# Performance work log

Measured on AMD Instinct MI355X. Metric: run time of the kernel, lower is better.

The kernel has to match this reference:

```python
import jax, jax.numpy as jnp
import numpy as np

NUM_EMBEDDINGS = 512
EMBEDDING_DIM = 64
BETA = 0.25


def setup_inputs() -> dict:
    key = jax.random.key(0)
    k1, k2 = jax.random.split(key)
    latent_z = jax.random.normal(k1, (32, EMBEDDING_DIM, 64, 64), dtype=jnp.float32)
    # nn.Embedding init: uniform(-1/K, 1/K)
    scale = 1.0 / NUM_EMBEDDINGS
    embedding = jax.random.uniform(k2, (NUM_EMBEDDINGS, EMBEDDING_DIM), dtype=jnp.float32,
                                   minval=-scale, maxval=scale)
    return {"latent_z": latent_z, "embedding": embedding}


def reference(latent_z, embedding):
    # [B, C, H, W] -> [B, H, W, C]
    z = jnp.transpose(latent_z, (0, 2, 3, 1))
    B, H, W, D = z.shape
    flat_z = z.reshape(-1, D)  # [N, D]

    # squared L2 distances via expansion: ||z||^2 + ||e||^2 - 2 z.e
    dist = (jnp.sum(flat_z ** 2, axis=1, keepdims=True)
            + jnp.sum(embedding ** 2, axis=1)
            - 2.0 * flat_z @ embedding.T)  # [N, K]

    idx = jnp.argmin(dist, axis=1)  # [N]
    encodings = jax.nn.one_hot(idx, NUM_EMBEDDINGS, dtype=flat_z.dtype)  # [N, K]

    # gather codes (same math as one_hot @ embedding)
    quantized = embedding[idx].reshape(B, H, W, D)

    quant_loss = (jnp.mean((jax.lax.stop_gradient(quantized) - z) ** 2)
                  + BETA * jnp.mean((quantized - jax.lax.stop_gradient(z)) ** 2))

    # straight-through estimator
    quantized_st = z + jax.lax.stop_gradient(quantized - z)

    mean_enc = jnp.mean(encodings, axis=0)
    perplexity = jnp.exp(-jnp.sum(mean_enc * jnp.log(mean_enc + 1e-10)))

    quantized_out = jnp.transpose(quantized_st, (0, 3, 1, 2))  # back to [B, C, H, W]
    return quant_loss, quantized_out, perplexity, encodings, idx[:, None]
```

## Files before the change

kernel.cpp:

```cpp
#include <hip/hip_runtime.h>
#include <math.h>

#define NPIX   131072
#define KCODES 512
#define DIM    64
#define HW     4096
#define CHW    262144
#define NBLK   1024

#define O_Q    1ll
#define O_PERP 8388609ll
#define O_ENC  8388610ll
#define O_IDX  75497474ll


__device__ __forceinline__ float np_sumsq64(const float (&x)[64]) {
#pragma clang fp contract(off)
  float r0 = x[0]*x[0], r1 = x[1]*x[1], r2 = x[2]*x[2], r3 = x[3]*x[3];
  float r4 = x[4]*x[4], r5 = x[5]*x[5], r6 = x[6]*x[6], r7 = x[7]*x[7];
#pragma unroll
  for (int i = 8; i < 64; i += 8) {
    r0 += x[i+0]*x[i+0];
    r1 += x[i+1]*x[i+1];
    r2 += x[i+2]*x[i+2];
    r3 += x[i+3]*x[i+3];
    r4 += x[i+4]*x[i+4];
    r5 += x[i+5]*x[i+5];
    r6 += x[i+6]*x[i+6];
    r7 += x[i+7]*x[i+7];
  }
  return ((r0+r1)+(r2+r3))+((r4+r5)+(r6+r7));
}

__global__ void vq_prep(const float* __restrict__ emb, float* __restrict__ ws) {
  const int t = threadIdx.x;
  if (t == 0) ws[0] = 0.0f;
  ((unsigned*)ws)[1 + t] = 0u;
  float x[64];
  const float* e = emb + t * DIM;
#pragma unroll
  for (int d = 0; d < 64; ++d) x[d] = e[d];
  ws[513 + t] = np_sumsq64(x);
}


__device__ __forceinline__ void et_prefetch8(const float* __restrict__ emb,
                                             int g, int ec, int eh, float4& p0) {
  const float* er = emb + (size_t)(256 * (g >> 3) + ec) * 64
                        + 8 * (g & 7) + 4 * eh;
  p0 = *(const float4*)er;
}

__device__ __forceinline__ void et_write8(float* __restrict__ ETb,
                                          const float4& p0, int eh, int ec) {
  const float tmp[4] = {p0.x, p0.y, p0.z, p0.w};
#pragma unroll
  for (int dl = 0; dl < 4; ++dl) ETb[(4 * eh + dl) * 256 + ec] = tmp[dl];
}

__device__ __forceinline__ void enc_zero(float2* __restrict__ encb, int batch, int t) {
  const float2 zz = make_float2(0.0f, 0.0f);
#pragma unroll
  for (int u = 0; u < 8; ++u)
    encb[(size_t)batch * 4096 + u * 512 + t] = zz;
}

__device__ __forceinline__ void dl_loop8(const float* __restrict__ ETb,
                                         const float* __restrict__ zl,
                                         int sdim, int pi, int ci,
                                         float (&acc)[8][8]) {
#pragma unroll 2
  for (int dl = 0; dl < 8; ++dl) {
    const float* zp = &zl[(sdim + dl) * 128 + 8 * pi];
    const float4 za0 = *(const float4*)(zp + 0);
    const float4 za1 = *(const float4*)(zp + 4);
    const float* ep = &ETb[dl * 256 + 4 * ci];
    const float4 e0 = *(const float4*)(ep + 0);
    const float4 e1 = *(const float4*)(ep + 128);
    const float zr[8] = {za0.x, za0.y, za0.z, za0.w,
                         za1.x, za1.y, za1.z, za1.w};
    const float er_[8] = {e0.x, e0.y, e0.z, e0.w,
                          e1.x, e1.y, e1.z, e1.w};
#pragma unroll
    for (int j = 0; j < 8; ++j)
#pragma unroll
      for (int c = 0; c < 8; ++c)
        acc[j][c] = fmaf(zr[j], er_[c], acc[j][c]);
  }
}

__device__ __forceinline__ void dist_phase(int Hh, int ci, int pi,
                                           const float (&acc)[8][8],
                                           const float* __restrict__ esq_l,
                                           const float* __restrict__ zsq_l,
                                           float (&bd)[8], int (&bk)[8]) {
#pragma unroll
  for (int q = 0; q < 2; ++q)
#pragma unroll
    for (int r = 0; r < 4; ++r) {
      const int k = 256 * Hh + 128 * q + 4 * ci + r;
      const float eq = esq_l[k];
#pragma unroll
      for (int j = 0; j < 8; ++j) {
        const float dist = (zsq_l[8 * pi + j] + eq) - 2.0f * acc[j][4 * q + r];
        if (dist < bd[j]) { bd[j] = dist; bk[j] = k; }
      }
    }
}

__global__ __launch_bounds__(512, 4)
void vq_main(
    const float* __restrict__ z, const float* __restrict__ emb,
    float* __restrict__ out, float* __restrict__ ws)
{
  __shared__ float ET_s[2][8 * 256];
  __shared__ float z_l[64 * 128];
  __shared__ float esq_l[512];
  __shared__ float zsq_l[128];
  __shared__ int   ridx_l[128];
  __shared__ float wsum[8];

  const int t   = threadIdx.x;
  const int ci  = t & 31;
  const int pi  = t >> 5;
  const int blk = blockIdx.x;
  const int n0  = blk * 128;
  const int b   = n0 >> 12;
  const int hw0 = n0 & 4095;
  const float* zg = z + (size_t)b * CHW + hw0;

  esq_l[t] = ws[513 + t];

  {
    const int i     = t & 31;
    const int dbase = t >> 5;
#pragma unroll
    for (int r = 0; r < 4; ++r) {
      const int d = dbase + 16 * r;
      *(float4*)&z_l[d * 128 + 4 * i] = *(const float4*)(zg + (size_t)d * HW + 4 * i);
    }
  }

  const int ec = t & 255;
  const int eh = t >> 8;
  float4 p0;
  et_prefetch8(emb, 0, ec, eh, p0);

  __syncthreads();

  if (t < 128) {
    float x[64];
#pragma unroll
    for (int d = 0; d < 64; ++d) x[d] = z_l[d * 128 + t];
    zsq_l[t] = np_sumsq64(x);
  }

  et_write8(&ET_s[0][0], p0, eh, ec);
  et_prefetch8(emb, 1, ec, eh, p0);

  __syncthreads();

  float bd[8];
  int   bk[8];
#pragma unroll
  for (int j = 0; j < 8; ++j) { bd[j] = INFINITY; bk[j] = 0; }
  float acc[8][8];
#pragma unroll
  for (int j = 0; j < 8; ++j)
#pragma unroll
    for (int c = 0; c < 8; ++c) acc[j][c] = 0.0f;

  float2* encb = (float2*)(out + O_ENC) + (size_t)n0 * 256;

  for (int g = 0; g < 16; ++g) {
    if (g < 15) et_write8(&ET_s[(g + 1) & 1][0], p0, eh, ec);
    if (g < 14) et_prefetch8(emb, g + 2, ec, eh, p0);
    if (!(g & 1)) enc_zero(encb, g >> 1, t);
    dl_loop8(&ET_s[g & 1][0], z_l, 8 * (g & 7), pi, ci, acc);
    if ((g & 7) == 7) {
      dist_phase(g >> 3, ci, pi, acc, esq_l, zsq_l, bd, bk);
      if (g == 7) {
#pragma unroll
        for (int j = 0; j < 8; ++j)
#pragma unroll
          for (int c = 0; c < 8; ++c) acc[j][c] = 0.0f;
      }
    }
    __syncthreads();
  }

#pragma unroll
  for (int m = 16; m >= 1; m >>= 1) {
#pragma unroll
    for (int j = 0; j < 8; ++j) {
      const float od = __shfl_xor(bd[j], m, 64);
      const int   ok = __shfl_xor(bk[j], m, 64);
      if (od < bd[j] || (od == bd[j] && ok < bk[j])) { bd[j] = od; bk[j] = ok; }
    }
  }
  if (ci == 0) {
#pragma unroll
    for (int j = 0; j < 8; ++j) ridx_l[8 * pi + j] = bk[j];
  }
  __syncthreads();

  if (t < 128) {
    const int k = ridx_l[t];
    out[O_IDX + n0 + t] = (float)k;
    atomicAdd((unsigned*)ws + 1 + k, 1u);
    out[O_ENC + (size_t)(n0 + t) * 512 + k] = 1.0f;
  }

  {
    const int px = t & 127;
    const int dq = t >> 7;
    const int k  = ridx_l[px];
    const float* e0 = emb + ((size_t)k << 6);
    float* q0 = out + O_Q + (size_t)b * CHW + hw0 + px;
    float lsum = 0.0f;
#pragma unroll
    for (int j = 0; j < 16; ++j) {
      const int d = dq * 16 + j;
      const float ev = e0[d];
      const float df = ev - z_l[d * 128 + px];
      lsum = fmaf(df, df, lsum);
      q0[(size_t)d * HW] = ev;
    }
#pragma unroll
    for (int off = 32; off > 0; off >>= 1) lsum += __shfl_down(lsum, off, 64);
    if ((t & 63) == 0) wsum[t >> 6] = lsum;
  }
  __syncthreads();
  if (t == 0)
    atomicAdd(ws, ((wsum[0] + wsum[1]) + (wsum[2] + wsum[3])) +
                  ((wsum[4] + wsum[5]) + (wsum[6] + wsum[7])));
}

__global__ void vq_fin(float* __restrict__ out, const float* __restrict__ ws) {
  __shared__ float red[8];
  const int t = threadIdx.x;
  const unsigned* counts = (const unsigned*)ws + 1;
  const float p = (float)counts[t] * (1.0f / 131072.0f);
  float h = p * logf(p + 1e-10f);
#pragma unroll
  for (int off = 32; off > 0; off >>= 1) h += __shfl_down(h, off, 64);
  if ((t & 63) == 0) red[t >> 6] = h;
  __syncthreads();
  if (t == 0) {
    float H = 0.0f;
#pragma unroll
    for (int w = 0; w < 8; ++w) H += red[w];
    out[O_PERP] = expf(-H);
    out[0] = 1.25f * ws[0] * (1.0f / 8388608.0f);
  }
}

extern "C" void kernel_launch(void* const* d_in, const int* in_sizes, int n_in,
                              void* d_out, int out_size, void* d_ws, size_t ws_size,
                              hipStream_t stream) {
  const float* z   = (const float*)d_in[0];
  const float* emb = (const float*)d_in[1];
  float* out = (float*)d_out;
  float* ws  = (float*)d_ws;

  vq_prep<<<1, 512, 0, stream>>>(emb, ws);
  vq_main<<<NBLK, 512, 0, stream>>>(z, emb, out, ws);
  vq_fin<<<1, 512, 0, stream>>>(out, ws);
}
```

Before: 445.4 us.

## Stage transposed codebook in workspace and load tiles via direct global-to-LDS loads

The prep kernel now also writes a transposed copy of the embedding into the workspace. The main kernel fills the z tile and the codebook tiles with global_load_lds DMA straight into shared memory, instead of going through registers and scattered LDS stores. The codebook K-step is doubled to 16 dims per stage, halving the number of barriers and loop trips, and s_setprio is raised around the FMA loop. In exchange there is more LDS per block, which may reduce occupancy, and the kernel now depends on async LDS load semantics. The diff ends mid-loop, so whether waits are inserted correctly before each barrier is unclear.

```diff
diff --git a/kernel.cpp b/kernel.cpp
--- a/kernel.cpp
+++ b/kernel.cpp
@@ -13,6 +13,11 @@
 #define O_ENC  8388610ll
 #define O_IDX  75497474ll
 
+#define WS_EMBT 1280
+
+#define GLD16(gp, lp) __builtin_amdgcn_global_load_lds( \
+    (const __attribute__((address_space(1))) unsigned int*)(gp), \
+    (__attribute__((address_space(3))) unsigned int*)(lp), 16, 0, 0)
 
 __device__ __forceinline__ float np_sumsq64(const float (&x)[64]) {
 #pragma clang fp contract(off)
@@ -41,36 +46,36 @@
 #pragma unroll
   for (int d = 0; d < 64; ++d) x[d] = e[d];
   ws[513 + t] = np_sumsq64(x);
-}
-
-
-__device__ __forceinline__ void et_prefetch8(const float* __restrict__ emb,
-                                             int g, int ec, int eh, float4& p0) {
-  const float* er = emb + (size_t)(256 * (g >> 3) + ec) * 64
-                        + 8 * (g & 7) + 4 * eh;
-  p0 = *(const float4*)er;
-}
-
-__device__ __forceinline__ void et_write8(float* __restrict__ ETb,
-                                          const float4& p0, int eh, int ec) {
-  const float tmp[4] = {p0.x, p0.y, p0.z, p0.w};
-#pragma unroll
-  for (int dl = 0; dl < 4; ++dl) ETb[(4 * eh + dl) * 256 + ec] = tmp[dl];
-}
-
-__device__ __forceinline__ void enc_zero(float2* __restrict__ encb, int batch, int t) {
+#pragma unroll
+  for (int d = 0; d < 64; ++d) ws[WS_EMBT + d * 512 + t] = x[d];
+}
+
+
+__device__ __forceinline__ void issue_ET(const float* __restrict__ embT,
+                                         float* __restrict__ dstbuf,
+                                         int g, int wv, int lane) {
+#pragma unroll
+  for (int q = 0; q < 2; ++q) {
+    const int r = 2 * wv + q;
+    const float* gp = embT + (size_t)((g & 3) * 16 + r) * 512
+                    + 256 * (g >> 2) + 4 * lane;
+    GLD16(gp, dstbuf + r * 256);
+  }
+}
+
+__device__ __forceinline__ void enc_zero(float2* __restrict__ encb, int g, int t) {
   const float2 zz = make_float2(0.0f, 0.0f);
 #pragma unroll
   for (int u = 0; u < 8; ++u)
-    encb[(size_t)batch * 4096 + u * 512 + t] = zz;
-}
-
-__device__ __forceinline__ void dl_loop8(const float* __restrict__ ETb,
-                                         const float* __restrict__ zl,
-                                         int sdim, int pi, int ci,
-                                         float (&acc)[8][8]) {
+    encb[(size_t)g * 4096 + u * 512 + t] = zz;
+}
+
+__device__ __forceinline__ void dl_loop(const float* __restrict__ ETb,
+                                        const float* __restrict__ zl,
+                                        int sdim, int pi, int ci,
+                                        float (&acc)[8][8]) {
 #pragma unroll 2
-  for (int dl = 0; dl < 8; ++dl) {
+  for (int dl = 0; dl < 16; ++dl) {
     const float* zp = &zl[(sdim + dl) * 128 + 8 * pi];
     const float4 za0 = *(const float4*)(zp + 0);
     const float4 za1 = *(const float4*)(zp + 4);
@@ -113,38 +118,35 @@
     const float* __restrict__ z, const float* __restrict__ emb,
     float* __restrict__ out, float* __restrict__ ws)
 {
-  __shared__ float ET_s[2][8 * 256];
+  __shared__ float ET_s[2][16 * 256];
   __shared__ float z_l[64 * 128];
   __shared__ float esq_l[512];
   __shared__ float zsq_l[128];
   __shared__ int   ridx_l[128];
   __shared__ float wsum[8];
 
-  const int t   = threadIdx.x;
-  const int ci  = t & 31;
-  const int pi  = t >> 5;
-  const int blk = blockIdx.x;
-  const int n0  = blk * 128;
-  const int b   = n0 >> 12;
-  const int hw0 = n0 & 4095;
-  const float* zg = z + (size_t)b * CHW + hw0;
+  const int t    = threadIdx.x;
+  const int lane = t & 63;
+  const int wv   = t >> 6;
+  const int ci   = t & 31;
+  const int pi   = t >> 5;
+  const int blk  = blockIdx.x;
+  const int n0   = blk * 128;
+  const int b    = n0 >> 12;
+  const int hw0  = n0 & 4095;
+  const float* zg   = z + (size_t)b * CHW + hw0;
+  const float* embT = ws + WS_EMBT;
 
   esq_l[t] = ws[513 + t];
 
-  {
-    const int i     = t & 31;
-    const int dbase = t >> 5;
-#pragma unroll
-    for (int r = 0; r < 4; ++r) {
-      const int d = dbase + 16 * r;
-      *(float4*)&z_l[d * 128 + 4 * i] = *(const float4*)(zg + (size_t)d * HW + 4 * i);
-    }
-  }
-
-  const int ec = t & 255;
-  const int eh = t >> 8;
-  float4 p0;
-  et_prefetch8(emb, 0, ec, eh, p0);
+#pragma unroll
+  for (int c = 0; c < 4; ++c) {
+    const int d0 = 2 * (4 * wv + c);
+    const float* gp = zg + (size_t)(d0 + (lane >> 5)) * HW + 4 * (lane & 31);
+    GLD16(gp, &z_l[d0 * 128]);
+  }
+
+  issue_ET(embT, &ET_s[0][0], 0, wv, lane);
 
   __syncthreads();
 
@@ -155,11 +157,6 @@
     zsq_l[t] = np_sumsq64(x);
   }
 
-  et_write8(&ET_s[0][0], p0, eh, ec);
-  et_prefetch8(emb, 1, ec, eh, p0);
-
-  __syncthreads();
-
   float bd[8];
   int   bk[8];
 #pragma unroll
@@ -172,14 +169,15 @@
 
   float2* encb = (float2*)(out + O_ENC) + (size_t)n0 * 256;
 
-  for (int g = 0; g < 16; ++g) {
-    if (g < 15) et_write8(&ET_s[(g + 1) & 1][0], p0, eh, ec);
-    if (g < 14) et_prefetch8(emb, g + 2, ec, eh, p0);
-    if (!(g & 1)) enc_zero(encb, g >> 1, t);
-    dl_loop8(&ET_s[g & 1][0], z_l, 8 * (g & 7), pi, ci, acc);
-    if ((g & 7) == 7) {
-      dist_phase(g >> 3, ci, pi, acc, esq_l, zsq_l, bd, bk);
-      if (g == 7) {
+  for (int g = 0; g < 8; ++g) {
+    if (g < 7) issue_ET(embT, &ET_s[(g + 1) & 1][0], g + 1, wv, lane);
+    enc_zero(encb, g, t);
+    __builtin_amdgcn_s_setprio(1);
+    dl_loop(&ET_s[g & 1][0], z_l, 16 * (g & 3), pi, ci, acc);
+    __builtin_amdgcn_s_setprio(0);
+    if ((g & 3) == 3) {
+      dist_phase(g >> 2, ci, pi, acc, esq_l, zsq_l, bd, bk);
+      if (g == 3) {
 #pragma unroll
         for (int j = 0; j < 8; ++j)
 #pragma unroll
```

After: 433.5 us. 1.03x faster.
